# Kernel tuning notes

Hardware: AMD Instinct MI355X
Metric: run time of the kernel (lower is better)

Reference implementation:

```python
import jax, jax.numpy as jnp
import numpy as np

C = 512
GROUPS = 32
EPS = 1e-6


def setup_inputs() -> dict:
    key = jax.random.key(0)
    ks = jax.random.split(key, 12)
    B, H, W = 4, 64, 64
    s = 1.0 / np.sqrt(C)
    return {
        "x": jax.random.normal(ks[0], (B, C, H, W), dtype=jnp.float32),
        "gn_w": jnp.ones((C,), jnp.float32),
        "gn_b": jnp.zeros((C,), jnp.float32),
        "wq": jax.random.normal(ks[1], (C, C), jnp.float32) * s,
        "bq": jnp.zeros((C,), jnp.float32),
        "wk": jax.random.normal(ks[2], (C, C), jnp.float32) * s,
        "bk": jnp.zeros((C,), jnp.float32),
        "wv": jax.random.normal(ks[3], (C, C), jnp.float32) * s,
        "bv": jnp.zeros((C,), jnp.float32),
        "wp": jax.random.normal(ks[4], (C, C), jnp.float32) * s,
        "bp": jnp.zeros((C,), jnp.float32),
    }


def _group_norm(x, w, b):
    B, Cc, H, W = x.shape
    xg = x.reshape(B, GROUPS, Cc // GROUPS, H, W)
    mu = xg.mean(axis=(2, 3, 4), keepdims=True)
    var = xg.var(axis=(2, 3, 4), keepdims=True)
    xg = (xg - mu) * jax.lax.rsqrt(var + EPS)
    xn = xg.reshape(B, Cc, H, W)
    return xn * w[None, :, None, None] + b[None, :, None, None]


def _conv1x1(x, w, b):
    # x: (B,C,H,W), w: (O,C) -> (B,O,H,W)
    return jnp.einsum('bchw,oc->bohw', x, w) + b[None, :, None, None]


def reference(x, gn_w, gn_b, wq, bq, wk, bk, wv, bv, wp, bp):
    B, Cc, H, W = x.shape
    N = H * W
    scale = Cc ** (-0.5)
    h_ = _group_norm(x, gn_w, gn_b)
    q = _conv1x1(h_, wq, bq).reshape(B, Cc, N)  # (B,C,N)
    k = _conv1x1(h_, wk, bk).reshape(B, Cc, N)
    v = _conv1x1(h_, wv, bv).reshape(B, Cc, N)
    # scores[b,i,j] = sum_c q[b,c,i] * k[b,c,j]
    attn = jnp.einsum('bci,bcj->bij', q, k) * scale  # (B,N,N)
    attn = jax.nn.softmax(attn, axis=2)
    # h_[b,c,i] = sum_j v[b,c,j] * attn[b,i,j]
    h2 = jnp.einsum('bcj,bij->bci', v, attn).reshape(B, Cc, H, W)
    return x + _conv1x1(h2, wp, bp)
```

## Files before the change

kernel.cpp:

```cpp
#include <hip/hip_runtime.h>

#define NPIX 4096
#define CCH  512
#define NGRP 32
#define BATCH 4
#define NT   64

using bf16 = __bf16;
typedef __bf16 bf16x8 __attribute__((ext_vector_type(8)));
typedef __bf16 bf16x4 __attribute__((ext_vector_type(4)));
typedef float  f32x4  __attribute__((ext_vector_type(4)));

__device__ __forceinline__ f32x4 mfma16(bf16x8 a, bf16x8 b, f32x4 c) {
    return __builtin_amdgcn_mfma_f32_16x16x32_bf16(a, b, c, 0, 0, 0);
}

__device__ __forceinline__ void gld_lds16(const void* g, void* l) {
    __builtin_amdgcn_global_load_lds(
        (const __attribute__((address_space(1))) unsigned int*)g,
        (__attribute__((address_space(3))) unsigned int*)l,
        16, 0, 0);
}

__device__ __forceinline__ void swz_src(int l, int& drow, int& dcol) {
    int m = (l & 7) ^ (l >> 3);
    drow = 2 * (l >> 3) + (m >> 2);
    dcol = (m & 3) * 8;
}
__device__ __forceinline__ int swz_roff(int c, int g) {
    return ((c >> 1) << 6) + ((((((c & 1) << 2) | g)) ^ ((c >> 1) & 7)) << 3);
}

__global__ __launch_bounds__(256) void cvt_all(const float* __restrict__ wq,
                                               const float* __restrict__ wk,
                                               const float* __restrict__ wv,
                                               const float* __restrict__ wp,
                                               bf16* __restrict__ d, float cscale) {
    int i = blockIdx.x * 256 + threadIdx.x;
    int seg = i >> 16;
    const float* s = (seg == 0) ? wq : (seg == 1) ? wk : (seg == 2) ? wv : wp;
    float scale = (seg == 0) ? cscale : 1.f;
    float4 v = ((const float4*)s)[i & 65535];
    bf16x4 o;
    o[0] = (bf16)(v.x*scale); o[1] = (bf16)(v.y*scale);
    o[2] = (bf16)(v.z*scale); o[3] = (bf16)(v.w*scale);
    ((bf16x4*)d)[i] = o;
}

__global__ __launch_bounds__(256) void gn_stats(const float* __restrict__ x, float2* __restrict__ stats) {
    int bg = blockIdx.x;
    const float4* p = (const float4*)(x + (size_t)bg * 65536);
    float s = 0.f, ss = 0.f;
    for (int i = threadIdx.x; i < 16384; i += 256) {
        float4 v = p[i];
        s  += v.x + v.y + v.z + v.w;
        ss += v.x*v.x + v.y*v.y + v.z*v.z + v.w*v.w;
    }
    __shared__ float r1[256], r2[256];
    int t = threadIdx.x;
    r1[t] = s; r2[t] = ss;
    __syncthreads();
    for (int st = 128; st > 0; st >>= 1) {
        if (t < st) { r1[t] += r1[t+st]; r2[t] += r2[t+st]; }
        __syncthreads();
    }
    if (t == 0) {
        float mu  = r1[0] * (1.f/65536.f);
        float var = r2[0] * (1.f/65536.f) - mu*mu;
        stats[bg] = make_float2(mu, rsqrtf(var + 1e-6f));
    }
}

__global__ __launch_bounds__(256) void gn_norm_t(const float* __restrict__ x,
                                                 const float2* __restrict__ stats,
                                                 const float* __restrict__ gw,
                                                 const float* __restrict__ gb,
                                                 bf16* __restrict__ hnt) {
    __shared__ float tile[64][65];
    int n0 = blockIdx.x * 64, c0 = blockIdx.y * 64, b = blockIdx.z;
    int t = threadIdx.x;
    {
        int cr = t >> 4;
        int nc = (t & 15) * 4;
        #pragma unroll
        for (int rep = 0; rep < 4; ++rep) {
            int c = c0 + rep*16 + cr;
            float2 st = stats[b*NGRP + (c >> 4)];
            float w = gw[c], bb = gb[c];
            float4 v = *(const float4*)(x + ((size_t)b*CCH + c)*NPIX + n0 + nc);
            float* dst = &tile[rep*16 + cr][nc];
            dst[0] = (v.x - st.x)*st.y*w + bb;
            dst[1] = (v.y - st.x)*st.y*w + bb;
            dst[2] = (v.z - st.x)*st.y*w + bb;
            dst[3] = (v.w - st.x)*st.y*w + bb;
        }
    }
    __syncthreads();
    {
        int nr = t >> 2;
        int cp = (t & 3) * 16;
        bf16x8 o0, o1;
        #pragma unroll
        for (int j = 0; j < 8; ++j) {
            o0[j] = (bf16)tile[cp + j    ][nr];
            o1[j] = (bf16)tile[cp + 8 + j][nr];
        }
        bf16* dst = hnt + ((size_t)b*NPIX + n0 + nr)*CCH + c0 + cp;
        *(bf16x8*)dst       = o0;
        *((bf16x8*)dst + 1) = o1;
    }
}

__global__ __launch_bounds__(256, 2)
void gemm_qkv(const bf16* __restrict__ Wcat, const bf16* __restrict__ X,
              const float* __restrict__ bq, const float* __restrict__ bk,
              const float* __restrict__ bv, bf16* __restrict__ qt,
              bf16* __restrict__ kt, bf16* __restrict__ vch, float cscale) {
    __shared__ bf16 tX[2][4096];
    __shared__ bf16 tW[2][4096];
    int n0 = blockIdx.x * 128, o0g = blockIdx.y * 128, b = blockIdx.z;
    int seg = o0g >> 9, osel = o0g & 511;
    const float* bias = (seg == 0) ? bq : (seg == 1) ? bk : bv;
    bf16* Yb = (seg == 0) ? qt : (seg == 1) ? kt : vch;
    float osc = (seg == 0) ? cscale : 1.f;
    bool vmode = (seg == 2);

    int t = threadIdx.x, lane = t & 63, w = t >> 6;
    int wm = (w >> 1) * 64, wn = (w & 1) * 64;
    int col = lane & 15, g = lane >> 4;
    int roff = swz_roff(col, g);
    int drow, dcol;
    swz_src(lane, drow, dcol);
    f32x4 acc[4][4] = {};
    const bf16* gX = X + ((size_t)b*NPIX + n0) * CCH;
    const bf16* gW = Wcat + (size_t)o0g * CCH;

    auto stage = [&](int buf, int k0) {
        #pragma unroll
        for (int i = 0; i < 2; ++i) {
            int rb = (w*2 + i) * 16;
            gld_lds16(gX + (size_t)(rb + drow)*CCH + k0 + dcol, &tX[buf][rb*32]);
            gld_lds16(gW + (size_t)(rb + drow)*CCH + k0 + dcol, &tW[buf][rb*32]);
        }
    };

    stage(0, 0);
    __syncthreads();

    for (int it = 0; it < 16; ++it) {
        int buf = it & 1;
        if (it < 15) stage(buf ^ 1, (it + 1) * 32);
        bf16x8 fA[4], fB[4];
        #pragma unroll
        for (int i = 0; i < 4; ++i) {
            if (!vmode) {
                fA[i] = *(bf16x8*)&tX[buf][(wm + i*16)*32 + roff];
                fB[i] = *(bf16x8*)&tW[buf][(wn + i*16)*32 + roff];
            } else {
                fA[i] = *(bf16x8*)&tW[buf][(wm + i*16)*32 + roff];
                fB[i] = *(bf16x8*)&tX[buf][(wn + i*16)*32 + roff];
            }
        }
        #pragma unroll
        for (int i = 0; i < 4; ++i)
            #pragma unroll
            for (int j = 0; j < 4; ++j)
                acc[i][j] = mfma16(fA[i], fB[j], acc[i][j]);
        __syncthreads();
    }

    int row4 = g * 4;
    #pragma unroll
    for (int i = 0; i < 4; ++i) {
        #pragma unroll
        for (int j = 0; j < 4; ++j) {
            #pragma unroll
            for (int r = 0; r < 4; ++r) {
                float vv = acc[i][j][r];
                int m = wm + i*16 + row4 + r;
                int n = wn + j*16 + col;
                if (!vmode) {
                    int sp = n0 + m, o = osel + n;
                    Yb[((size_t)b*NPIX + sp)*CCH + o] = (bf16)(vv + osc*bias[o]);
                } else {
                    int o = osel + m, sp = n0 + n;
                    Yb[((size_t)b*CCH + o)*NPIX + sp] = (bf16)(vv + bias[o]);
                }
            }
        }
    }
}

__global__ __launch_bounds__(256, 2)
void gemm_proj(const bf16* __restrict__ W, const bf16* __restrict__ X,
               const float* __restrict__ bias, float* __restrict__ Yf,
               const float* __restrict__ resid) {
    __shared__ bf16 tX[2][4096];
    __shared__ bf16 tW[2][4096];
    int n0 = blockIdx.x * 128, o0 = blockIdx.y * 128, b = blockIdx.z;
    int t = threadIdx.x, lane = t & 63, w = t >> 6;
    int wm = (w >> 1) * 64, wn = (w & 1) * 64;
    int col = lane & 15, g = lane >> 4;
    int roff = swz_roff(col, g);
    int drow, dcol;
    swz_src(lane, drow, dcol);
    f32x4 acc[4][4] = {};
    const bf16* gX = X + ((size_t)b*NPIX + n0) * CCH;
    const bf16* gW = W + (size_t)o0 * CCH;

    auto stage = [&](int buf, int k0) {
        #pragma unroll
        for (int i = 0; i < 2; ++i) {
            int rb = (w*2 + i) * 16;
            gld_lds16(gX + (size_t)(rb + drow)*CCH + k0 + dcol, &tX[buf][rb*32]);
            gld_lds16(gW + (size_t)(rb + drow)*CCH + k0 + dcol, &tW[buf][rb*32]);
        }
    };

    stage(0, 0);
    __syncthreads();

    for (int it = 0; it < 16; ++it) {
        int buf = it & 1;
        if (it < 15) stage(buf ^ 1, (it + 1) * 32);
        bf16x8 fA[4], fB[4];
        #pragma unroll
        for (int i = 0; i < 4; ++i) {
            fA[i] = *(bf16x8*)&tW[buf][(wm + i*16)*32 + roff];
            fB[i] = *(bf16x8*)&tX[buf][(wn + i*16)*32 + roff];
        }
        #pragma unroll
        for (int i = 0; i < 4; ++i)
            #pragma unroll
            for (int j = 0; j < 4; ++j)
                acc[i][j] = mfma16(fA[i], fB[j], acc[i][j]);
        __syncthreads();
    }

    int row4 = g * 4;
    #pragma unroll
    for (int i = 0; i < 4; ++i) {
        #pragma unroll
        for (int j = 0; j < 4; ++j) {
            #pragma unroll
            for (int r = 0; r < 4; ++r) {
                int o = o0 + wm + i*16 + row4 + r;
                int sp = n0 + wn + j*16 + col;
                size_t idx = ((size_t)b*CCH + o)*NPIX + sp;
                Yf[idx] = acc[i][j][r] + bias[o] + resid[idx];
            }
        }
    }
}

__global__ __launch_bounds__(512, 2)
void attn_flash(const bf16* __restrict__ qt, const bf16* __restrict__ kt,
                const bf16* __restrict__ v, bf16* __restrict__ pacc0,
                bf16* __restrict__ pacc1, float* __restrict__ lsum) {
    __shared__ bf16 Kt[2][16384];
    __shared__ bf16 Vt[2][16384];
    __shared__ bf16 Pl[2][8][16][40];
    __shared__ float Ls[128];

    const int L  = blockIdx.x + 32 * blockIdx.y + 128 * blockIdx.z;
    const int gx = L & 7, ix = L >> 3;
    const int b  = gx & 3, jz = gx >> 2;

    const int t = threadIdx.x, lane = t & 63, w = t >> 6;
    const int q0 = ix * 128 + w * 16;
    const int col = lane & 15, g = lane >> 4, kq = g * 8;
    const int jbase = jz * 2048;

    const bf16* kbase = kt + (size_t)b*NPIX*CCH;
    const bf16* vbase = v  + (size_t)b*CCH*NPIX;
    int drow, dcol; swz_src(lane, drow, dcol);
    const int kx0 = (col & 7) << 4;
    const int vro = 2*swz_roff(col, g);

    bf16x8 qf[16];
    {
        const bf16* qrow = qt + ((size_t)b*NPIX + q0 + col)*CCH + kq;
        #pragma unroll
        for (int kk = 0; kk < 16; ++kk) qf[kk] = *(const bf16x8*)(qrow + kk*32);
    }

    auto stage = [&](int buf, int j0) {
        #pragma unroll
        for (int i = 0; i < 4; ++i) {
            int row = w*4 + i;
            gld_lds16((const char*)(kbase + (size_t)(j0 + row)*CCH) + ((lane*16) ^ ((row & 7) << 4)),
                      (char*)&Kt[buf][0] + row*1024);
        }
        #pragma unroll
        for (int i = 0; i < 4; ++i) {
            int blk = w*4 + i;
            gld_lds16(vbase + (size_t)(blk*16 + drow)*NPIX + j0 + dcol,
                      (char*)&Vt[buf][0] + blk*1024);
        }
    };

    f32x4 acc[8][4] = {};
    float lacc[4] = {0.f, 0.f, 0.f, 0.f};

    auto qkt_exp = [&](int buf) {
        f32x4 s0a = {}, s0b = {}, s1a = {}, s1b = {};
        const char* kb0 = (const char*)&Kt[buf][0] + col*1024;
        const char* kb1 = kb0 + 16*1024;
        #pragma unroll
        for (int kk = 0; kk < 16; kk += 2) {
            int e0 = (kk*64     + g*16) ^ kx0;
            int e1 = ((kk+1)*64 + g*16) ^ kx0;
            s0a = mfma16(qf[kk],   *(const bf16x8*)(kb0 + e0), s0a);
            s1a = mfma16(qf[kk],   *(const bf16x8*)(kb1 + e0), s1a);
            s0b = mfma16(qf[kk+1], *(const bf16x8*)(kb0 + e1), s0b);
            s1b = mfma16(qf[kk+1], *(const bf16x8*)(kb1 + e1), s1b);
        }
        f32x4 s0 = s0a + s0b;
        f32x4 s1 = s1a + s1b;
        #pragma unroll
        for (int r = 0; r < 4; ++r) {
            float p0 = __expf(s0[r]);
            float p1 = __expf(s1[r]);
            lacc[r] += p0 + p1;
            Pl[buf][w][g*4 + r][col]      = (bf16)p0;
            Pl[buf][w][g*4 + r][col + 16] = (bf16)p1;
        }
    };

    stage(0, jbase);
    __syncthreads();

    stage(1, jbase + 32);
    qkt_exp(0);
    __syncthreads();

    for (int it = 1; it < NT; ++it) {
        const int buf = it & 1, pb = buf ^ 1;

        const char* vb = (const char*)&Vt[pb][0] + (w << 12);
        bf16x8 bv0 = *(const bf16x8*)(vb          + vro);
        bf16x8 bv1 = *(const bf16x8*)(vb + 1024   + vro);
        bf16x8 bv2 = *(const bf16x8*)(vb + 2048   + vro);
        bf16x8 bv3 = *(const bf16x8*)(vb + 3072   + vro);
        asm volatile("s_waitcnt lgkmcnt(0)" ::: "memory");
        __builtin_amdgcn_sched_barrier(0);

        if (it < NT-1) stage(pb, jbase + (it + 1) * 32);

        #pragma unroll
        for (int qtl = 0; qtl < 8; ++qtl) {
            bf16x8 pa = *(bf16x8*)&Pl[pb][qtl][col][kq];
            acc[qtl][0] = mfma16(pa, bv0, acc[qtl][0]);
            acc[qtl][1] = mfma16(pa, bv1, acc[qtl][1]);
            acc[qtl][2] = mfma16(pa, bv2, acc[qtl][2]);
            acc[qtl][3] = mfma16(pa, bv3, acc[qtl][3]);
        }

        qkt_exp(buf);
        __syncthreads();
    }

    {
        const char* vb = (const char*)&Vt[1][0] + (w << 12);
        bf16x8 bv0 = *(const bf16x8*)(vb          + vro);
        bf16x8 bv1 = *(const bf16x8*)(vb + 1024   + vro);
        bf16x8 bv2 = *(const bf16x8*)(vb + 2048   + vro);
        bf16x8 bv3 = *(const bf16x8*)(vb + 3072   + vro);
        #pragma unroll
        for (int qtl = 0; qtl < 8; ++qtl) {
            bf16x8 pa = *(bf16x8*)&Pl[1][qtl][col][kq];
            acc[qtl][0] = mfma16(pa, bv0, acc[qtl][0]);
            acc[qtl][1] = mfma16(pa, bv1, acc[qtl][1]);
            acc[qtl][2] = mfma16(pa, bv2, acc[qtl][2]);
            acc[qtl][3] = mfma16(pa, bv3, acc[qtl][3]);
        }
    }

    #pragma unroll
    for (int r = 0; r < 4; ++r) {
        float s = lacc[r];
        #pragma unroll
        for (int off = 1; off < 16; off <<= 1) s += __shfl_xor(s, off);
        if (col == 0) {
            Ls[w*16 + g*4 + r] = 1.f / s;
            lsum[((size_t)jz*BATCH + b)*NPIX + q0 + g*4 + r] = s;
        }
    }
    __syncthreads();

    bf16* pout = jz ? pacc1 : pacc0;
    const int q0b = ix * 128;
    #pragma unroll
    for (int qtl = 0; qtl < 8; ++qtl) {
        f32x4 rlq = *(const f32x4*)&Ls[qtl*16 + g*4];
        #pragma unroll
        for (int i = 0; i < 4; ++i) {
            int ch = w*64 + i*16 + col;
            bf16x4 ov;
            #pragma unroll
            for (int r = 0; r < 4; ++r) ov[r] = (bf16)(acc[qtl][i][r] * rlq[r]);
            *(bf16x4*)(pout + ((size_t)b*CCH + ch)*NPIX + q0b + qtl*16 + g*4) = ov;
        }
    }
}

__global__ __launch_bounds__(256)
void merge_t(const bf16* __restrict__ p0, const bf16* __restrict__ p1,
             const float* __restrict__ lsum, bf16* __restrict__ h2t) {
    __shared__ float tile[64][65];
    __shared__ float w0s[64], w1s[64];
    int n0 = blockIdx.x * 64, c0 = blockIdx.y * 64, b = blockIdx.z;
    int t = threadIdx.x;
    if (t < 64) {
        float l0 = lsum[(size_t)b*NPIX + n0 + t];
        float l1 = lsum[(size_t)(BATCH + b)*NPIX + n0 + t];
        float inv = 1.f / (l0 + l1);
        w0s[t] = l0 * inv; w1s[t] = l1 * inv;
    }
    __syncthreads();
    {
        int cl = t >> 2, nc = (t & 3) * 16;
        size_t base = ((size_t)b*CCH + c0 + cl)*NPIX + n0 + nc;
        #pragma unroll
        for (int h = 0; h < 2; ++h) {
            bf16x8 a0 = *(const bf16x8*)(p0 + base + h*8);
            bf16x8 a1 = *(const bf16x8*)(p1 + base + h*8);
            #pragma unroll
            for (int j = 0; j < 8; ++j)
                tile[cl][nc + h*8 + j] = (float)a0[j]*w0s[nc + h*8 + j]
                                       + (float)a1[j]*w1s[nc + h*8 + j];
        }
    }
    __syncthreads();
    {
        int nr = t >> 2, cp = (t & 3) * 16;
        bf16x8 o0, o1;
        #pragma unroll
        for (int j = 0; j < 8; ++j) {
            o0[j] = (bf16)tile[cp + j    ][nr];
            o1[j] = (bf16)tile[cp + 8 + j][nr];
        }
        bf16* dst = h2t + ((size_t)b*NPIX + n0 + nr)*CCH + c0 + cp;
        *(bf16x8*)dst       = o0;
        *((bf16x8*)dst + 1) = o1;
    }
}

extern "C" void kernel_launch(void* const* d_in, const int* in_sizes, int n_in,
                              void* d_out, int out_size, void* d_ws, size_t ws_size,
                              hipStream_t stream) {
    (void)in_sizes; (void)n_in; (void)out_size; (void)ws_size;
    const float* x   = (const float*)d_in[0];
    const float* gnw = (const float*)d_in[1];
    const float* gnb = (const float*)d_in[2];
    const float* wq  = (const float*)d_in[3];
    const float* bq  = (const float*)d_in[4];
    const float* wk  = (const float*)d_in[5];
    const float* bk  = (const float*)d_in[6];
    const float* wv  = (const float*)d_in[7];
    const float* bv  = (const float*)d_in[8];
    const float* wp  = (const float*)d_in[9];
    const float* bp  = (const float*)d_in[10];
    const float cscale = 0.04419417382415922f;

    char* ws = (char*)d_ws;
    bf16* wcat = (bf16*)ws;
    bf16* wpb  = wcat + 3*262144;
    float2* stats = (float2*)(ws + 4*524288);
    const size_t TEN = (size_t)BATCH*NPIX*CCH;
    bf16* hnt = (bf16*)(ws + 4*524288 + 4096);
    bf16* qt  = hnt + TEN;
    bf16* kt  = qt  + TEN;
    bf16* vch = kt  + TEN;
    bf16* pacc1 = vch + TEN;
    float* lsum = (float*)(pacc1 + TEN);
    bf16* pacc0 = hnt;
    bf16* h2t   = qt;

    cvt_all<<<1024, 256, 0, stream>>>(wq, wk, wv, wp, wcat, cscale);

    gn_stats<<<BATCH*NGRP, 256, 0, stream>>>(x, stats);
    gn_norm_t<<<dim3(NPIX/64, CCH/64, BATCH), 256, 0, stream>>>(x, stats, gnw, gnb, hnt);

    gemm_qkv<<<dim3(NPIX/128, 12, BATCH), 256, 0, stream>>>(
        wcat, hnt, bq, bk, bv, qt, kt, vch, cscale);

    attn_flash<<<dim3(32, BATCH, 2), 512, 0, stream>>>(qt, kt, vch, pacc0, pacc1, lsum);

    merge_t<<<dim3(NPIX/64, CCH/64, BATCH), 256, 0, stream>>>(pacc0, pacc1, lsum, h2t);

    gemm_proj<<<dim3(NPIX/128, CCH/128, BATCH), 256, 0, stream>>>(
        wpb, h2t, bp, (float*)d_out, x);
}
```

Measured before the change: 293.5 us.

## Split GN stats into more partial blocks and stagger K/V staging in attention

```diff
diff --git a/kernel.cpp b/kernel.cpp
--- a/kernel.cpp
+++ b/kernel.cpp
@@ -47,32 +47,30 @@
     ((bf16x4*)d)[i] = o;
 }
 
-__global__ __launch_bounds__(256) void gn_stats(const float* __restrict__ x, float2* __restrict__ stats) {
-    int bg = blockIdx.x;
-    const float4* p = (const float4*)(x + (size_t)bg * 65536);
+__global__ __launch_bounds__(256) void gn_part(const float* __restrict__ x,
+                                               float2* __restrict__ partials) {
+    int blk = blockIdx.x;
+    const float4* p = (const float4*)(x + (size_t)(blk >> 3) * 65536 + (blk & 7) * 8192);
     float s = 0.f, ss = 0.f;
-    for (int i = threadIdx.x; i < 16384; i += 256) {
-        float4 v = p[i];
+    int t = threadIdx.x;
+    #pragma unroll
+    for (int i = 0; i < 8; ++i) {
+        float4 v = p[t + i*256];
         s  += v.x + v.y + v.z + v.w;
         ss += v.x*v.x + v.y*v.y + v.z*v.z + v.w*v.w;
     }
     __shared__ float r1[256], r2[256];
-    int t = threadIdx.x;
     r1[t] = s; r2[t] = ss;
     __syncthreads();
     for (int st = 128; st > 0; st >>= 1) {
         if (t < st) { r1[t] += r1[t+st]; r2[t] += r2[t+st]; }
         __syncthreads();
     }
-    if (t == 0) {
-        float mu  = r1[0] * (1.f/65536.f);
-        float var = r2[0] * (1.f/65536.f) - mu*mu;
-        stats[bg] = make_float2(mu, rsqrtf(var + 1e-6f));
-    }
+    if (t == 0) partials[blk] = make_float2(r1[0], r2[0]);
 }
 
 __global__ __launch_bounds__(256) void gn_norm_t(const float* __restrict__ x,
-                                                 const float2* __restrict__ stats,
+                                                 const float2* __restrict__ partials,
                                                  const float* __restrict__ gw,
                                                  const float* __restrict__ gb,
                                                  bf16* __restrict__ hnt) {
@@ -85,14 +83,22 @@
         #pragma unroll
         for (int rep = 0; rep < 4; ++rep) {
             int c = c0 + rep*16 + cr;
-            float2 st = stats[b*NGRP + (c >> 4)];
+            int grp = b*NGRP + (c >> 4);
+            float s = 0.f, ss = 0.f;
+            #pragma unroll
+            for (int k = 0; k < 8; ++k) {
+                float2 pp = partials[grp*8 + k];
+                s += pp.x; ss += pp.y;
+            }
+            float mu   = s * (1.f/65536.f);
+            float rsig = rsqrtf(ss * (1.f/65536.f) - mu*mu + 1e-6f);
             float w = gw[c], bb = gb[c];
             float4 v = *(const float4*)(x + ((size_t)b*CCH + c)*NPIX + n0 + nc);
             float* dst = &tile[rep*16 + cr][nc];
-            dst[0] = (v.x - st.x)*st.y*w + bb;
-            dst[1] = (v.y - st.x)*st.y*w + bb;
-            dst[2] = (v.z - st.x)*st.y*w + bb;
-            dst[3] = (v.w - st.x)*st.y*w + bb;
+            dst[0] = (v.x - mu)*rsig*w + bb;
+            dst[1] = (v.y - mu)*rsig*w + bb;
+            dst[2] = (v.z - mu)*rsig*w + bb;
+            dst[3] = (v.w - mu)*rsig*w + bb;
         }
     }
     __syncthreads();
@@ -284,13 +290,15 @@
         for (int kk = 0; kk < 16; ++kk) qf[kk] = *(const bf16x8*)(qrow + kk*32);
     }
 
-    auto stage = [&](int buf, int j0) {
+    auto stage_K = [&](int buf, int j0) {
         #pragma unroll
         for (int i = 0; i < 4; ++i) {
             int row = w*4 + i;
             gld_lds16((const char*)(kbase + (size_t)(j0 + row)*CCH) + ((lane*16) ^ ((row & 7) << 4)),
                       (char*)&Kt[buf][0] + row*1024);
         }
+    };
+    auto stage_V = [&](int buf, int j0) {
         #pragma unroll
         for (int i = 0; i < 4; ++i) {
             int blk = w*4 + i;
@@ -327,26 +335,12 @@
         }
     };
 
-    stage(0, jbase);
-    __syncthreads();
-
-    stage(1, jbase + 32);
-    qkt_exp(0);
-    __syncthreads();
-
-    for (int it = 1; it < NT; ++it) {
-        const int buf = it & 1, pb = buf ^ 1;
-
+    auto pv = [&](int pb) {
         const char* vb = (const char*)&Vt[pb][0] + (w << 12);
         bf16x8 bv0 = *(const bf16x8*)(vb          + vro);
         bf16x8 bv1 = *(const bf16x8*)(vb + 1024   + vro);
         bf16x8 bv2 = *(const bf16x8*)(vb + 2048   + vro);
         bf16x8 bv3 = *(const bf16x8*)(vb + 3072   + vro);
-        asm volatile("s_waitcnt lgkmcnt(0)" ::: "memory");
-        __builtin_amdgcn_sched_barrier(0);
-
-        if (it < NT-1) stage(pb, jbase + (it + 1) * 32);
-
         #pragma unroll
         for (int qtl = 0; qtl < 8; ++qtl) {
             bf16x8 pa = *(bf16x8*)&Pl[pb][qtl][col][kq];
@@ -355,26 +349,32 @@
             acc[qtl][2] = mfma16(pa, bv2, acc[qtl][2]);
             acc[qtl][3] = mfma16(pa, bv3, acc[qtl][3]);
         }
+    };
+
+    stage_K(0, jbase);
+    stage_V(0, jbase);
+    __syncthreads();
+
+    stage_K(1, jbase + 32);
+    stage_V(1, jbase + 32);
+    qkt_exp(0);
+    __syncthreads();
+
+    for (int it = 1; it < NT; ++it) {
+        const int buf = it & 1, pb = buf ^ 1;
+
+        if (it < NT-1) stage_K(pb, jbase + (it + 1) * 32);
+
+        pv(pb);
+
+        asm volatile("s_waitcnt lgkmcnt(0)" ::: "memory");
+        if (it < NT-1) stage_V(pb, jbase + (it + 1) * 32);
 
         qkt_exp(buf);
         __syncthreads();
     }
 
-    {
-        const char* vb = (const char*)&Vt[1][0] + (w << 12);
-        bf16x8 bv0 = *(const bf16x8*)(vb          + vro);
-        bf16x8 bv1 = *(const bf16x8*)(vb + 1024   + vro);
-        bf16x8 bv2 = *(const bf16x8*)(vb + 2048   + vro);
-        bf16x8 bv3 = *(const bf16x8*)(vb + 3072   + vro);
-        #pragma unroll
-        for (int qtl = 0; qtl < 8; ++qtl) {
-            bf16x8 pa = *(bf16x8*)&Pl[1][qtl][col][kq];
-            acc[qtl][0] = mfma16(pa, bv0, acc[qtl][0]);
-            acc[qtl][1] = mfma16(pa, bv1, acc[qtl][1]);
-            acc[qtl][2] = mfma16(pa, bv2, acc[qtl][2]);
-            acc[qtl][3] = mfma16(pa, bv3, acc[qtl][3]);
-        }
-    }
+    pv(1);
 
     #pragma unroll
     for (int r = 0; r < 4; ++r) {
@@ -466,9 +466,9 @@
     char* ws = (char*)d_ws;
     bf16* wcat = (bf16*)ws;
     bf16* wpb  = wcat + 3*262144;
-    float2* stats = (float2*)(ws + 4*524288);
+    float2* partials = (float2*)(ws + 4*524288);
     const size_t TEN = (size_t)BATCH*NPIX*CCH;
-    bf16* hnt = (bf16*)(ws + 4*524288 + 4096);
+    bf16* hnt = (bf16*)(ws + 4*524288 + 16384);
     bf16* qt  = hnt + TEN;
     bf16* kt  = qt  + TEN;
     bf16* vch = kt  + TEN;
@@ -479,8 +479,8 @@
 
     cvt_all<<<1024, 256, 0, stream>>>(wq, wk, wv, wp, wcat, cscale);
 
-    gn_stats<<<BATCH*NGRP, 256, 0, stream>>>(x, stats);
-    gn_norm_t<<<dim3(NPIX/64, CCH/64, BATCH), 256, 0, stream>>>(x, stats, gnw, gnb, hnt);
+    gn_part<<<1024, 256, 0, stream>>>(x, partials);
+    gn_norm_t<<<dim3(NPIX/64, CCH/64, BATCH), 256, 0, stream>>>(x, partials, gnw, gnb, hnt);
 
     gemm_qkv<<<dim3(NPIX/128, 12, BATCH), 256, 0, stream>>>(
         wcat, hnt, bq, bk, bv, qt, kt, vch, cscale);
```

New measurement: 303.1 us. +3.3%, slower.
